# Kernel optimization log

Measured on AMD Instinct MI355X. Metric: run time of the kernel, lower is better.

The kernel has to match this reference:

```python
import jax, jax.numpy as jnp
import numpy as np

B, T, C, HP, WP = 2, 8, 384, 128, 128
WS = 8
NH = 12  # num_heads
EPS = 1e-5


def setup_inputs() -> dict:
    key = jax.random.key(0)
    ks = jax.random.split(key, 9)
    s = 0.02
    return {
        "x": jax.random.normal(ks[0], (B, T, C, HP, WP), jnp.float32),
        "norm_gamma": jnp.ones((C,), jnp.float32),
        "norm_beta": jnp.zeros((C,), jnp.float32),
        "in_proj_w": jax.random.normal(ks[1], (3 * C, C), jnp.float32) * s,
        "in_proj_b": jnp.zeros((3 * C,), jnp.float32),
        "out_proj_w": jax.random.normal(ks[2], (C, C), jnp.float32) * s,
        "out_proj_b": jnp.zeros((C,), jnp.float32),
        "proj_w": jax.random.normal(ks[3], (C, C), jnp.float32) * s,
        "proj_b": jnp.zeros((C,), jnp.float32),
    }


def reference(x, norm_gamma, norm_beta, in_proj_w, in_proj_b,
              out_proj_w, out_proj_b, proj_w, proj_b):
    b, t, c, hp, wp = x.shape
    ws = WS
    nh, nw = hp // ws, wp // ws
    dh = c // NH

    # window partition: (B,T,C,H,W) -> (B*T*nH*nW, ws*ws, C)
    xw = jnp.transpose(x, (0, 1, 3, 4, 2))                # (B,T,H,W,C)
    xw = xw.reshape(b * t, nh, ws, nw, ws, c)
    xw = jnp.transpose(xw, (0, 1, 3, 2, 4, 5))            # (BT,nH,nW,ws,ws,C)
    xw = xw.reshape(b * t * nh * nw, ws * ws, c)          # (N,S,C)

    # LayerNorm over channel dim
    mu = jnp.mean(xw, axis=-1, keepdims=True)
    var = jnp.mean((xw - mu) ** 2, axis=-1, keepdims=True)
    xn = (xw - mu) * jax.lax.rsqrt(var + EPS) * norm_gamma + norm_beta

    # fused QKV projection (torch MHA in_proj layout: rows are [q;k;v])
    qkv = jnp.einsum('nsc,dc->nsd', xn, in_proj_w) + in_proj_b
    q, k, v = jnp.split(qkv, 3, axis=-1)
    n, s = q.shape[0], q.shape[1]
    q = q.reshape(n, s, NH, dh)
    k = k.reshape(n, s, NH, dh)
    v = v.reshape(n, s, NH, dh)

    scale = 1.0 / np.sqrt(dh).astype(np.float32)
    attn = jnp.einsum('nqhd,nkhd->nhqk', q * scale, k)
    attn = jax.nn.softmax(attn, axis=-1)
    o = jnp.einsum('nhqk,nkhd->nqhd', attn, v).reshape(n, s, c)

    # MHA out_proj then extra proj
    o = jnp.einsum('nsc,dc->nsd', o, out_proj_w) + out_proj_b
    o = jnp.einsum('nsc,dc->nsd', o, proj_w) + proj_b

    # window merge back to (B,T,C,H,W)
    o = o.reshape(b * t, nh, nw, ws, ws, c)
    o = jnp.transpose(o, (0, 1, 3, 2, 4, 5)).reshape(b, t, hp, wp, c)
    return jnp.transpose(o, (0, 1, 4, 2, 3))
```

## Files before the change

### kernel.cpp

```cpp
#include <hip/hip_runtime.h>

#define C_    384
#define NH_   12
#define DH_   32
#define HPX   128
#define WPX   128
#define NWIN_ 4096
#define TOK_  262144

typedef __attribute__((ext_vector_type(8))) short short8;
typedef __attribute__((ext_vector_type(4))) float f32x4;

__device__ __forceinline__ unsigned short f2bf(float f) {
  unsigned u = __builtin_bit_cast(unsigned, f);
  u = (u + 0x7fffu + ((u >> 16) & 1u)) >> 16;
  return (unsigned short)u;
}

__global__ __launch_bounds__(256) void prep_kernel(
    const float* __restrict__ in_w, const float* __restrict__ op_w,
    const float* __restrict__ op_b, const float* __restrict__ p_w,
    const float* __restrict__ p_b, unsigned short* __restrict__ wqkv,
    unsigned short* __restrict__ wf, float* __restrict__ bfv)
{
  int tid = blockIdx.x * blockDim.x + threadIdx.x;
  int stride = gridDim.x * blockDim.x;
  for (int i = tid; i < 3 * C_ * C_; i += stride) wqkv[i] = f2bf(in_w[i]);
  for (int i = tid; i < C_ * C_; i += stride) {
    int r = i / C_, c = i % C_;
    float acc = 0.f;
    for (int k = 0; k < C_; k++) acc += p_w[r * C_ + k] * op_w[k * C_ + c];
    wf[i] = f2bf(acc);
  }
  for (int i = tid; i < C_; i += stride) {
    float acc = p_b[i];
    for (int k = 0; k < C_; k++) acc += p_w[i * C_ + k] * op_b[k];
    bfv[i] = acc;
  }
}

__global__ __launch_bounds__(256) void fused_attn(
    const float* __restrict__ x, const float* __restrict__ gamma,
    const float* __restrict__ beta, const unsigned short* __restrict__ wqkv,
    const float* __restrict__ bqkv, unsigned short* __restrict__ o1)
{
  __shared__ char smem[61440];
  char* xnb = smem;
  char* Qb  = smem + 49152;
  char* Kb  = smem + 53248;
  char* VTb = smem + 57344;
  char* Pb  = smem + 49152;
  float* red   = (float*)(smem + 49152);
  float* stats = (float*)(smem + 49152 + 2048);

  const int win = (blockIdx.x & 7) * (NWIN_ / 8) + (blockIdx.x >> 3);
  const int bt = win >> 8, wh = (win >> 4) & 15, ww = win & 15;
  const int tid = threadIdx.x;
  const int w = tid >> 6, l = tid & 63;
  const int l15 = l & 15, sub = l >> 4;

  const float* xb = x + ((size_t)bt * C_ * HPX + (size_t)wh * 8) * WPX + ww * 8;
  const int i0 = l >> 3, j0 = l & 7;

  float sm = 0.f, sq = 0.f;
  for (int c = w; c < C_; c += 4) {
    float v = xb[(size_t)c * (HPX * WPX) + i0 * WPX + j0];
    sm += v; sq += v * v;
  }
  red[(w * 64 + l) * 2] = sm;
  red[(w * 64 + l) * 2 + 1] = sq;
  __syncthreads();
  if (tid < 64) {
    float a0 = 0.f, a1 = 0.f;
    for (int p = 0; p < 4; p++) { a0 += red[(p * 64 + tid) * 2]; a1 += red[(p * 64 + tid) * 2 + 1]; }
    float mu = a0 * (1.f / C_);
    float var = a1 * (1.f / C_) - mu * mu;
    stats[tid * 2] = mu;
    stats[tid * 2 + 1] = rsqrtf(var + 1e-5f);
  }
  __syncthreads();
  const float mu = stats[l * 2], rsg = stats[l * 2 + 1];

  for (int c = w; c < C_; c += 4) {
    float v = xb[(size_t)c * (HPX * WPX) + i0 * WPX + j0];
    float xv = (v - mu) * rsg * gamma[c] + beta[c];
    unsigned byte = (unsigned)(l * 768 + c * 2) ^ (unsigned)((l & 7) << 4);
    *(unsigned short*)(xnb + byte) = f2bf(xv);
  }
  __syncthreads();

  const int mw = w >> 1, nw = w & 1;
  const float scale = 0.1767766952966369f;
  const f32x4 zf = {0.f, 0.f, 0.f, 0.f};

  for (int h = 0; h < NH_; h++) {
    int wr[3];
    #pragma unroll
    for (int jj = 0; jj < 3; jj++) {
      int j = 3 * nw + jj;
      wr[jj] = (j >> 1) * C_ + h * DH_ + (j & 1) * 16;
    }
    f32x4 acc[2][3];
    #pragma unroll
    for (int r = 0; r < 2; r++)
      #pragma unroll
      for (int jj = 0; jj < 3; jj++) acc[r][jj] = zf;

    for (int kc = 0; kc < 12; kc++) {
      short8 a[2];
      #pragma unroll
      for (int r = 0; r < 2; r++) {
        int tok = 32 * mw + 16 * r + l15;
        unsigned byte = (unsigned)(tok * 768 + kc * 64 + (sub << 4)) ^ (unsigned)((tok & 7) << 4);
        a[r] = *(const short8*)(xnb + byte);
      }
      #pragma unroll
      for (int jj = 0; jj < 3; jj++) {
        short8 b = *(const short8*)(wqkv + ((size_t)(wr[jj] + l15) * C_ + kc * 32 + (sub << 3)));
        acc[0][jj] = __builtin_amdgcn_mfma_f32_16x16x32_bf16(a[0], b, acc[0][jj], 0, 0, 0);
        acc[1][jj] = __builtin_amdgcn_mfma_f32_16x16x32_bf16(a[1], b, acc[1][jj], 0, 0, 0);
      }
    }
    __syncthreads();

    #pragma unroll
    for (int jj = 0; jj < 3; jj++) {
      int j = 3 * nw + jj;
      int typ = j >> 1;
      int dloc = (j & 1) * 16 + l15;
      float bias = bqkv[wr[jj] + l15];
      #pragma unroll
      for (int r = 0; r < 2; r++) {
        #pragma unroll
        for (int rr = 0; rr < 4; rr++) {
          int tok = 32 * mw + 16 * r + (sub << 2) + rr;
          float v = acc[r][jj][rr] + bias;
          if (typ == 0) {
            v *= scale;
            unsigned byte = (unsigned)(tok * 64 + dloc * 2) ^ (unsigned)((tok & 7) << 4);
            *(unsigned short*)(Qb + byte) = f2bf(v);
          } else if (typ == 1) {
            unsigned byte = (unsigned)(tok * 64 + dloc * 2) ^ (unsigned)((tok & 7) << 4);
            *(unsigned short*)(Kb + byte) = f2bf(v);
          } else {
            unsigned byte = (unsigned)(dloc * 128 + tok * 2) ^ (unsigned)((dloc & 7) << 4);
            *(unsigned short*)(VTb + byte) = f2bf(v);
          }
        }
      }
    }
    __syncthreads();

    short8 qa;
    {
      int tok = 16 * w + l15;
      unsigned byte = (unsigned)(tok * 64 + (sub << 4)) ^ (unsigned)((tok & 7) << 4);
      qa = *(const short8*)(Qb + byte);
    }
    f32x4 sacc[4];
    #pragma unroll
    for (int ct = 0; ct < 4; ct++) {
      int kt = ct * 16 + l15;
      unsigned byte = (unsigned)(kt * 64 + (sub << 4)) ^ (unsigned)((kt & 7) << 4);
      short8 kb = *(const short8*)(Kb + byte);
      sacc[ct] = __builtin_amdgcn_mfma_f32_16x16x32_bf16(qa, kb, zf, 0, 0, 0);
    }
    float inv[4];
    #pragma unroll
    for (int rr = 0; rr < 4; rr++) {
      float m = fmaxf(fmaxf(sacc[0][rr], sacc[1][rr]), fmaxf(sacc[2][rr], sacc[3][rr]));
      m = fmaxf(m, __shfl_xor(m, 1));
      m = fmaxf(m, __shfl_xor(m, 2));
      m = fmaxf(m, __shfl_xor(m, 4));
      m = fmaxf(m, __shfl_xor(m, 8));
      float s = 0.f;
      #pragma unroll
      for (int ct = 0; ct < 4; ct++) {
        float p = __expf(sacc[ct][rr] - m);
        sacc[ct][rr] = p;
        s += p;
      }
      s += __shfl_xor(s, 1); s += __shfl_xor(s, 2);
      s += __shfl_xor(s, 4); s += __shfl_xor(s, 8);
      inv[rr] = 1.0f / s;
    }
    __syncthreads();
    #pragma unroll
    for (int ct = 0; ct < 4; ct++)
      #pragma unroll
      for (int rr = 0; rr < 4; rr++) {
        int q = 16 * w + (sub << 2) + rr;
        int kk = ct * 16 + l15;
        unsigned byte = (unsigned)(q * 128 + kk * 2) ^ (unsigned)((q & 7) << 4);
        *(unsigned short*)(Pb + byte) = f2bf(sacc[ct][rr]);
      }
    __syncthreads();

    f32x4 oacc[2] = {zf, zf};
    #pragma unroll
    for (int kc = 0; kc < 2; kc++) {
      int q = 16 * w + l15;
      unsigned pb = (unsigned)(q * 128 + kc * 64 + (sub << 4)) ^ (unsigned)((q & 7) << 4);
      short8 pa = *(const short8*)(Pb + pb);
      #pragma unroll
      for (int dt = 0; dt < 2; dt++) {
        int d = dt * 16 + l15;
        unsigned vb = (unsigned)(d * 128 + kc * 64 + (sub << 4)) ^ (unsigned)((d & 7) << 4);
        short8 vv = *(const short8*)(VTb + vb);
        oacc[dt] = __builtin_amdgcn_mfma_f32_16x16x32_bf16(pa, vv, oacc[dt], 0, 0, 0);
      }
    }
    #pragma unroll
    for (int dt = 0; dt < 2; dt++)
      #pragma unroll
      for (int rr = 0; rr < 4; rr++) {
        int q = 16 * w + (sub << 2) + rr;
        int col = h * DH_ + dt * 16 + l15;
        o1[(size_t)(win * 64 + q) * C_ + col] = f2bf(oacc[dt][rr] * inv[rr]);
      }
  }
}

__global__ __launch_bounds__(256) void final_gemm(
    const unsigned short* __restrict__ o1, const unsigned short* __restrict__ wf,
    const float* __restrict__ bfv, float* __restrict__ out)
{
  __shared__ char smem[32768];
  char* As = smem;
  char* Bs = smem + 16384;

  const int blk = blockIdx.x;
  const int nt = blk % 3, mt = blk / 3;
  const int mbase = mt * 128, nbase = nt * 128;
  const int tid = threadIdx.x;
  const int w = tid >> 6, l = tid & 63;
  const int l15 = l & 15, sub = l >> 4;
  const int wm = w >> 1, wn = w & 1;
  const f32x4 zf = {0.f, 0.f, 0.f, 0.f};

  f32x4 acc[4][4];
  #pragma unroll
  for (int r = 0; r < 4; r++)
    #pragma unroll
    for (int c = 0; c < 4; c++) acc[r][c] = zf;

  for (int kb = 0; kb < C_; kb += 64) {
    __syncthreads();
    #pragma unroll
    for (int it = 0; it < 4; it++) {
      int row = it * 32 + (tid >> 3);
      int seg = tid & 7;
      unsigned byte = (unsigned)(row * 128 + seg * 16) ^ (unsigned)((row & 7) << 4);
      short8 va = *(const short8*)(o1 + (size_t)(mbase + row) * C_ + kb + seg * 8);
      *(short8*)(As + byte) = va;
      short8 vb = *(const short8*)(wf + (size_t)(nbase + row) * C_ + kb + seg * 8);
      *(short8*)(Bs + byte) = vb;
    }
    __syncthreads();
    #pragma unroll
    for (int kc = 0; kc < 2; kc++) {
      short8 a[4], b[4];
      #pragma unroll
      for (int r = 0; r < 4; r++) {
        int row = wm * 64 + r * 16 + l15;
        unsigned byte = (unsigned)(row * 128 + kc * 64 + (sub << 4)) ^ (unsigned)((row & 7) << 4);
        a[r] = *(const short8*)(As + byte);
      }
      #pragma unroll
      for (int c = 0; c < 4; c++) {
        int row = wn * 64 + c * 16 + l15;
        unsigned byte = (unsigned)(row * 128 + kc * 64 + (sub << 4)) ^ (unsigned)((row & 7) << 4);
        b[c] = *(const short8*)(Bs + byte);
      }
      #pragma unroll
      for (int r = 0; r < 4; r++)
        #pragma unroll
        for (int c = 0; c < 4; c++)
          acc[r][c] = __builtin_amdgcn_mfma_f32_16x16x32_bf16(a[r], b[c], acc[r][c], 0, 0, 0);
    }
  }

  #pragma unroll
  for (int r = 0; r < 4; r++) {
    int t0 = mbase + wm * 64 + r * 16 + (sub << 2);
    int win = t0 >> 6, s0 = t0 & 63;
    int bt = win >> 8, wh = (win >> 4) & 15, ww = win & 15;
    int ii = s0 >> 3, jj = s0 & 7;
    #pragma unroll
    for (int c4 = 0; c4 < 4; c4++) {
      int c = nbase + wn * 64 + c4 * 16 + l15;
      float bias = bfv[c];
      f32x4 v;
      v[0] = acc[r][c4][0] + bias;
      v[1] = acc[r][c4][1] + bias;
      v[2] = acc[r][c4][2] + bias;
      v[3] = acc[r][c4][3] + bias;
      size_t off = (((size_t)bt * C_ + c) * HPX + wh * 8 + ii) * WPX + ww * 8 + jj;
      *(f32x4*)(out + off) = v;
    }
  }
}

extern "C" void kernel_launch(void* const* d_in, const int* in_sizes, int n_in,
                              void* d_out, int out_size, void* d_ws, size_t ws_size,
                              hipStream_t stream)
{
  (void)in_sizes; (void)n_in; (void)out_size; (void)ws_size;
  const float* x     = (const float*)d_in[0];
  const float* gamma = (const float*)d_in[1];
  const float* beta  = (const float*)d_in[2];
  const float* in_w  = (const float*)d_in[3];
  const float* in_b  = (const float*)d_in[4];
  const float* op_w  = (const float*)d_in[5];
  const float* op_b  = (const float*)d_in[6];
  const float* p_w   = (const float*)d_in[7];
  const float* p_b   = (const float*)d_in[8];
  float* out = (float*)d_out;
  char* ws = (char*)d_ws;

  const size_t o1_bytes = (size_t)TOK_ * C_ * 2;
  unsigned short* o1   = (unsigned short*)ws;
  unsigned short* wqkv = (unsigned short*)(ws + o1_bytes);
  unsigned short* wf   = (unsigned short*)(ws + o1_bytes + 884736);
  float*          bfv  = (float*)(ws + o1_bytes + 884736 + 294912);

  prep_kernel<<<1024, 256, 0, stream>>>(in_w, op_w, op_b, p_w, p_b, wqkv, wf, bfv);
  fused_attn<<<NWIN_, 256, 0, stream>>>(x, gamma, beta, wqkv, in_b, o1);
  final_gemm<<<2048 * 3, 256, 0, stream>>>(o1, wf, bfv, out);
}
```

Baseline: 2.186 ms.

## Split fused window attention into LN, tiled QKV GEMM, and per-window attention kernels

Replaces the single fused LN+QKV+attention kernel with three stages: a LayerNorm/window-partition kernel writing bf16 xn to workspace, a 128x128 LDS-tiled QKV GEMM writing Q (pre-scaled), K and transposed V, and a per-window attention kernel that reads them from global memory. The goal is to remove the per-head GEMM in the fused kernel that re-read weights straight from global memory without LDS tiling, and to raise occupancy. The work is processed in chunks sized to fit the workspace, and attention output overwrites xn in place. The cost is extra global round-trips for xn and QKV and possibly many kernel launches when the workspace is small.

New measurement: 1.883 ms. 13.9% less time.

```diff
diff --git a/kernel.cpp b/kernel.cpp
--- a/kernel.cpp
+++ b/kernel.cpp
@@ -39,17 +39,12 @@
   }
 }
 
-__global__ __launch_bounds__(256) void fused_attn(
+__global__ __launch_bounds__(256) void ln_win(
     const float* __restrict__ x, const float* __restrict__ gamma,
-    const float* __restrict__ beta, const unsigned short* __restrict__ wqkv,
-    const float* __restrict__ bqkv, unsigned short* __restrict__ o1)
-{
-  __shared__ char smem[61440];
+    const float* __restrict__ beta, unsigned short* __restrict__ xn)
+{
+  __shared__ char smem[51712];
   char* xnb = smem;
-  char* Qb  = smem + 49152;
-  char* Kb  = smem + 53248;
-  char* VTb = smem + 57344;
-  char* Pb  = smem + 49152;
   float* red   = (float*)(smem + 49152);
   float* stats = (float*)(smem + 49152 + 2048);
 
@@ -57,15 +52,15 @@
   const int bt = win >> 8, wh = (win >> 4) & 15, ww = win & 15;
   const int tid = threadIdx.x;
   const int w = tid >> 6, l = tid & 63;
-  const int l15 = l & 15, sub = l >> 4;
-
   const float* xb = x + ((size_t)bt * C_ * HPX + (size_t)wh * 8) * WPX + ww * 8;
-  const int i0 = l >> 3, j0 = l & 7;
+  const int px = (l >> 3) * WPX + (l & 7);
 
   float sm = 0.f, sq = 0.f;
-  for (int c = w; c < C_; c += 4) {
-    float v = xb[(size_t)c * (HPX * WPX) + i0 * WPX + j0];
-    sm += v; sq += v * v;
+  for (int cp = w; cp < 192; cp += 4) {
+    int c = cp * 2;
+    float v0 = xb[(size_t)c * (HPX * WPX) + px];
+    float v1 = xb[(size_t)(c + 1) * (HPX * WPX) + px];
+    sm += v0 + v1; sq += v0 * v0 + v1 * v1;
   }
   red[(w * 64 + l) * 2] = sm;
   red[(w * 64 + l) * 2 + 1] = sq;
@@ -81,149 +76,225 @@
   __syncthreads();
   const float mu = stats[l * 2], rsg = stats[l * 2 + 1];
 
-  for (int c = w; c < C_; c += 4) {
-    float v = xb[(size_t)c * (HPX * WPX) + i0 * WPX + j0];
-    float xv = (v - mu) * rsg * gamma[c] + beta[c];
+  for (int cp = w; cp < 192; cp += 4) {
+    int c = cp * 2;
+    float v0 = xb[(size_t)c * (HPX * WPX) + px];
+    float v1 = xb[(size_t)(c + 1) * (HPX * WPX) + px];
+    float y0 = (v0 - mu) * rsg * gamma[c] + beta[c];
+    float y1 = (v1 - mu) * rsg * gamma[c + 1] + beta[c + 1];
+    unsigned pk = (unsigned)f2bf(y0) | ((unsigned)f2bf(y1) << 16);
     unsigned byte = (unsigned)(l * 768 + c * 2) ^ (unsigned)((l & 7) << 4);
-    *(unsigned short*)(xnb + byte) = f2bf(xv);
+    *(unsigned*)(xnb + byte) = pk;
   }
   __syncthreads();
 
-  const int mw = w >> 1, nw = w & 1;
+  unsigned short* xg = xn + (size_t)win * (64 * C_);
+  #pragma unroll
+  for (int i = 0; i < 12; i++) {
+    unsigned g = (unsigned)(i * 4096 + tid * 16);
+    unsigned row = g / 768;
+    unsigned byte = g ^ ((row & 7) << 4);
+    short8 v = *(const short8*)(xnb + byte);
+    *(short8*)(xg + (g >> 1)) = v;
+  }
+}
+
+__global__ __launch_bounds__(256) void qkv_gemm(
+    const unsigned short* __restrict__ xn, const unsigned short* __restrict__ wqkv,
+    const float* __restrict__ bqkv, unsigned short* __restrict__ qs,
+    unsigned short* __restrict__ ksp, unsigned short* __restrict__ vt)
+{
+  __shared__ char smem[32768];
+  char* As = smem;
+  char* Bs = smem + 16384;
+
+  const int blk = blockIdx.x;
+  const int nt = blk % 9, mt = blk / 9;
+  const int mbase = mt * 128, nbase = nt * 128;
+  const int tid = threadIdx.x;
+  const int w = tid >> 6, l = tid & 63;
+  const int l15 = l & 15, sub = l >> 4;
+  const int wm = w >> 1, wn = w & 1;
+  const f32x4 zf = {0.f, 0.f, 0.f, 0.f};
   const float scale = 0.1767766952966369f;
+
+  f32x4 acc[4][4];
+  #pragma unroll
+  for (int r = 0; r < 4; r++)
+    #pragma unroll
+    for (int c = 0; c < 4; c++) acc[r][c] = zf;
+
+  for (int kb = 0; kb < C_; kb += 64) {
+    __syncthreads();
+    #pragma unroll
+    for (int it = 0; it < 4; it++) {
+      int row = it * 32 + (tid >> 3);
+      int seg = tid & 7;
+      unsigned byte = (unsigned)(row * 128 + seg * 16) ^ (unsigned)((row & 7) << 4);
+      short8 va = *(const short8*)(xn + (size_t)(mbase + row) * C_ + kb + seg * 8);
+      *(short8*)(As + byte) = va;
+      short8 vb = *(const short8*)(wqkv + (size_t)(nbase + row) * C_ + kb + seg * 8);
+      *(short8*)(Bs + byte) = vb;
+    }
+    __syncthreads();
+    #pragma unroll
+    for (int kc = 0; kc < 2; kc++) {
+      short8 a[4], b[4];
+      #pragma unroll
+      for (int r = 0; r < 4; r++) {
+        int row = wm * 64 + r * 16 + l15;
+        unsigned byte = (unsigned)(row * 128 + kc * 64 + (sub << 4)) ^ (unsigned)((row & 7) << 4);
+        a[r] = *(const short8*)(As + byte);
+      }
+      #pragma unroll
+      for (int c = 0; c < 4; c++) {
+        int row = wn * 64 + c * 16 + l15;
+        unsigned byte = (unsigned)(row * 128 + kc * 64 + (sub << 4)) ^ (unsigned)((row & 7) << 4);
+        b[c] = *(const short8*)(Bs + byte);
+      }
+      #pragma unroll
+      for (int r = 0; r < 4; r++)
+        #pragma unroll
+        for (int c = 0; c < 4; c++)
+          acc[r][c] = __builtin_amdgcn_mfma_f32_16x16x32_bf16(a[r], b[c], acc[r][c], 0, 0, 0);
+    }
+  }
+
+  const int typ = nt / 3;
+  #pragma unroll
+  for (int r = 0; r < 4; r++) {
+    int t0 = mbase + wm * 64 + r * 16 + (sub << 2);
+    #pragma unroll
+    for (int c4 = 0; c4 < 4; c4++) {
+      int dg = nbase + wn * 64 + c4 * 16 + l15;
+      float bias = bqkv[dg];
+      if (typ == 0) {
+        #pragma unroll
+        for (int reg = 0; reg < 4; reg++)
+          qs[(size_t)(t0 + reg) * C_ + dg] = f2bf((acc[r][c4][reg] + bias) * scale);
+      } else if (typ == 1) {
+        #pragma unroll
+        for (int reg = 0; reg < 4; reg++)
+          ksp[(size_t)(t0 + reg) * C_ + (dg - C_)] = f2bf(acc[r][c4][reg] + bias);
+      } else {
+        int vd = dg - 2 * C_;
+        int win_l = t0 >> 6, s0 = t0 & 63;
+        unsigned short b0 = f2bf(acc[r][c4][0] + bias);
+        unsigned short b1 = f2bf(acc[r][c4][1] + bias);
+        unsigned short b2 = f2bf(acc[r][c4][2] + bias);
+        unsigned short b3 = f2bf(acc[r][c4][3] + bias);
+        unsigned lo = (unsigned)b0 | ((unsigned)b1 << 16);
+        unsigned hi = (unsigned)b2 | ((unsigned)b3 << 16);
+        unsigned* p = (unsigned*)(vt + ((size_t)win_l * C_ + vd) * 64 + s0);
+        p[0] = lo; p[1] = hi;
+      }
+    }
+  }
+}
+
+__global__ __launch_bounds__(256, 4) void attn_win(
+    const unsigned short* __restrict__ qs, const unsigned short* __restrict__ ksp,
+    const unsigned short* __restrict__ vt, unsigned short* __restrict__ o1)
+{
+  __shared__ char Pall[32768];
+  const int win_l = blockIdx.x;
+  const int tid = threadIdx.x;
+  const int w = tid >> 6, l = tid & 63;
+  const int l15 = l & 15, sub = l >> 4;
+  char* Pb = Pall + w * 8192;
+  const unsigned short* qw = qs + (size_t)win_l * 64 * C_;
+  const unsigned short* kw = ksp + (size_t)win_l * 64 * C_;
+  const unsigned short* vw = vt + (size_t)win_l * C_ * 64;
+  unsigned short* ow = o1 + (size_t)win_l * 64 * C_;
   const f32x4 zf = {0.f, 0.f, 0.f, 0.f};
 
-  for (int h = 0; h < NH_; h++) {
-    int wr[3];
-    #pragma unroll
-    for (int jj = 0; jj < 3; jj++) {
-      int j = 3 * nw + jj;
-      wr[jj] = (j >> 1) * C_ + h * DH_ + (j & 1) * 16;
-    }
-    f32x4 acc[2][3];
-    #pragma unroll
-    for (int r = 0; r < 2; r++)
-      #pragma unroll
-      for (int jj = 0; jj < 3; jj++) acc[r][jj] = zf;
-
-    for (int kc = 0; kc < 12; kc++) {
-      short8 a[2];
-      #pragma unroll
-      for (int r = 0; r < 2; r++) {
-        int tok = 32 * mw + 16 * r + l15;
-        unsigned byte = (unsigned)(tok * 768 + kc * 64 + (sub << 4)) ^ (unsigned)((tok & 7) << 4);
-        a[r] = *(const short8*)(xnb + byte);
-      }
-      #pragma unroll
-      for (int jj = 0; jj < 3; jj++) {
-        short8 b = *(const short8*)(wqkv + ((size_t)(wr[jj] + l15) * C_ + kc * 32 + (sub << 3)));
-        acc[0][jj] = __builtin_amdgcn_mfma_f32_16x16x32_bf16(a[0], b, acc[0][jj], 0, 0, 0);
-        acc[1][jj] = __builtin_amdgcn_mfma_f32_16x16x32_bf16(a[1], b, acc[1][jj], 0, 0, 0);
-      }
-    }
-    __syncthreads();
-
-    #pragma unroll
-    for (int jj = 0; jj < 3; jj++) {
-      int j = 3 * nw + jj;
-      int typ = j >> 1;
-      int dloc = (j & 1) * 16 + l15;
-      float bias = bqkv[wr[jj] + l15];
-      #pragma unroll
-      for (int r = 0; r < 2; r++) {
-        #pragma unroll
-        for (int rr = 0; rr < 4; rr++) {
-          int tok = 32 * mw + 16 * r + (sub << 2) + rr;
-          float v = acc[r][jj][rr] + bias;
-          if (typ == 0) {
-            v *= scale;
-            unsigned byte = (unsigned)(tok * 64 + dloc * 2) ^ (unsigned)((tok & 7) << 4);
-            *(unsigned short*)(Qb + byte) = f2bf(v);
-          } else if (typ == 1) {
-            unsigned byte = (unsigned)(tok * 64 + dloc * 2) ^ (unsigned)((tok & 7) << 4);
-            *(unsigned short*)(Kb + byte) = f2bf(v);
-          } else {
-            unsigned byte = (unsigned)(dloc * 128 + tok * 2) ^ (unsigned)((dloc & 7) << 4);
-            *(unsigned short*)(VTb + byte) = f2bf(v);
+  for (int hh = 0; hh < 3; hh++) {
+    const int h = w + hh * 4;
+    short8 kf[4];
+    #pragma unroll
+    for (int ct = 0; ct < 4; ct++)
+      kf[ct] = *(const short8*)(kw + (size_t)(ct * 16 + l15) * C_ + h * DH_ + sub * 8);
+
+    #pragma unroll
+    for (int hf = 0; hf < 2; hf++) {
+      f32x4 sc[2][4];
+      #pragma unroll
+      for (int rt2 = 0; rt2 < 2; rt2++) {
+        int rt = hf * 2 + rt2;
+        short8 qf = *(const short8*)(qw + (size_t)(rt * 16 + l15) * C_ + h * DH_ + sub * 8);
+        #pragma unroll
+        for (int ct = 0; ct < 4; ct++)
+          sc[rt2][ct] = __builtin_amdgcn_mfma_f32_16x16x32_bf16(qf, kf[ct], zf, 0, 0, 0);
+      }
+      float inv[2][4];
+      #pragma unroll
+      for (int rt2 = 0; rt2 < 2; rt2++) {
+        #pragma unroll
+        for (int reg = 0; reg < 4; reg++) {
+          float m = fmaxf(fmaxf(sc[rt2][0][reg], sc[rt2][1][reg]),
+                          fmaxf(sc[rt2][2][reg], sc[rt2][3][reg]));
+          m = fmaxf(m, __shfl_xor(m, 1));
+          m = fmaxf(m, __shfl_xor(m, 2));
+          m = fmaxf(m, __shfl_xor(m, 4));
+          m = fmaxf(m, __shfl_xor(m, 8));
+          float s = 0.f;
+          #pragma unroll
+          for (int ct = 0; ct < 4; ct++) {
+            float p = __expf(sc[rt2][ct][reg] - m);
+            sc[rt2][ct][reg] = p;
+            s += p;
           }
+          s += __shfl_xor(s, 1); s += __shfl_xor(s, 2);
+          s += __shfl_xor(s, 4); s += __shfl_xor(s, 8);
+          inv[rt2][reg] = 1.0f / s;
         }
       }
-    }
-    __syncthreads();
-
-    short8 qa;
-    {
-      int tok = 16 * w + l15;
-      unsigned byte = (unsigned)(tok * 64 + (sub << 4)) ^ (unsigned)((tok & 7) << 4);
-      qa = *(const short8*)(Qb + byte);
-    }
-    f32x4 sacc[4];
-    #pragma unroll
-    for (int ct = 0; ct < 4; ct++) {
-      int kt = ct * 16 + l15;
-      unsigned byte = (unsigned)(kt * 64 + (sub << 4)) ^ (unsigned)((kt & 7) << 4);
-      short8 kb = *(const short8*)(Kb + byte);
-      sacc[ct] = __builtin_amdgcn_mfma_f32_16x16x32_bf16(qa, kb, zf, 0, 0, 0);
-    }
-    float inv[4];
-    #pragma unroll
-    for (int rr = 0; rr < 4; rr++) {
-      float m = fmaxf(fmaxf(sacc[0][rr], sacc[1][rr]), fmaxf(sacc[2][rr], sacc[3][rr]));
-      m = fmaxf(m, __shfl_xor(m, 1));
-      m = fmaxf(m, __shfl_xor(m, 2));
-      m = fmaxf(m, __shfl_xor(m, 4));
-      m = fmaxf(m, __shfl_xor(m, 8));
-      float s = 0.f;
-      #pragma unroll
-      for (int ct = 0; ct < 4; ct++) {
-        float p = __expf(sacc[ct][rr] - m);
-        sacc[ct][rr] = p;
-        s += p;
-      }
-      s += __shfl_xor(s, 1); s += __shfl_xor(s, 2);
-      s += __shfl_xor(s, 4); s += __shfl_xor(s, 8);
-      inv[rr] = 1.0f / s;
-    }
-    __syncthreads();
-    #pragma unroll
-    for (int ct = 0; ct < 4; ct++)
-      #pragma unroll
-      for (int rr = 0; rr < 4; rr++) {
-        int q = 16 * w + (sub << 2) + rr;
-        int kk = ct * 16 + l15;
-        unsigned byte = (unsigned)(q * 128 + kk * 2) ^ (unsigned)((q & 7) << 4);
-        *(unsigned short*)(Pb + byte) = f2bf(sacc[ct][rr]);
-      }
-    __syncthreads();
-
-    f32x4 oacc[2] = {zf, zf};
-    #pragma unroll
-    for (int kc = 0; kc < 2; kc++) {
-      int q = 16 * w + l15;
-      unsigned pb = (unsigned)(q * 128 + kc * 64 + (sub << 4)) ^ (unsigned)((q & 7) << 4);
-      short8 pa = *(const short8*)(Pb + pb);
-      #pragma unroll
-      for (int dt = 0; dt < 2; dt++) {
-        int d = dt * 16 + l15;
-        unsigned vb = (unsigned)(d * 128 + kc * 64 + (sub << 4)) ^ (unsigned)((d & 7) << 4);
-        short8 vv = *(const short8*)(VTb + vb);
-        oacc[dt] = __builtin_amdgcn_mfma_f32_16x16x32_bf16(pa, vv, oacc[dt], 0, 0, 0);
-      }
-    }
-    #pragma unroll
-    for (int dt = 0; dt < 2; dt++)
-      #pragma unroll
-      for (int rr = 0; rr < 4; rr++) {
-        int q = 16 * w + (sub << 2) + rr;
-        int col = h * DH_ + dt * 16 + l15;
-        o1[(size_t)(win * 64 + q) * C_ + col] = f2bf(oacc[dt][rr] * inv[rr]);
-      }
+      #pragma unroll
+      for (int rt2 = 0; rt2 < 2; rt2++)
+        #pragma unroll
+        for (int ct = 0; ct < 4; ct++)
+          #pragma unroll
+          for (int reg = 0; reg < 4; reg++) {
+            int q = (hf * 2 + rt2) * 16 + (sub << 2) + reg;
+            int k = ct * 16 + l15;
+            unsigned byte = (unsigned)(q * 128 + k * 2) ^ (unsigned)((q & 7) << 4);
+            *(unsigned short*)(Pb + byte) = f2bf(sc[rt2][ct][reg]);
+          }
+      f32x4 oa[2][2] = {{zf, zf}, {zf, zf}};
+      #pragma unroll
+      for (int kc = 0; kc < 2; kc++) {
+        short8 pa[2];
+        #pragma unroll
+        for (int rt2 = 0; rt2 < 2; rt2++) {
+          int q = (hf * 2 + rt2) * 16 + l15;
+          unsigned byte = (unsigned)(q * 128 + kc * 64 + (sub << 4)) ^ (unsigned)((q & 7) << 4);
+          pa[rt2] = *(const short8*)(Pb + byte);
+        }
+        #pragma unroll
+        for (int dt = 0; dt < 2; dt++) {
+          short8 b = *(const short8*)(vw + (size_t)(h * DH_ + dt * 16 + l15) * 64 + kc * 32 + sub * 8);
+          #pragma unroll
+          for (int rt2 = 0; rt2 < 2; rt2++)
+            oa[rt2][dt] = __builtin_amdgcn_mfma_f32_16x16x32_bf16(pa[rt2], b, oa[rt2][dt], 0, 0, 0);
+        }
+      }
+      #pragma unroll
+      for (int rt2 = 0; rt2 < 2; rt2++)
+        #pragma unroll
+        for (int dt = 0; dt < 2; dt++)
+          #pragma unroll
+          for (int reg = 0; reg < 4; reg++) {
+            int q = (hf * 2 + rt2) * 16 + (sub << 2) + reg;
+            ow[(size_t)q * C_ + h * DH_ + dt * 16 + l15] =
+                f2bf(oa[rt2][dt][reg] * inv[rt2][reg]);
+          }
+    }
   }
 }
 
 __global__ __launch_bounds__(256) void final_gemm(
     const unsigned short* __restrict__ o1, const unsigned short* __restrict__ wf,
-    const float* __restrict__ bfv, float* __restrict__ out)
+    const float* __restrict__ bfv, float* __restrict__ out, int winBase)
 {
   __shared__ char smem[32768];
   char* As = smem;
@@ -283,7 +354,7 @@
   #pragma unroll
   for (int r = 0; r < 4; r++) {
     int t0 = mbase + wm * 64 + r * 16 + (sub << 2);
-    int win = t0 >> 6, s0 = t0 & 63;
+    int win = winBase + (t0 >> 6), s0 = t0 & 63;
     int bt = win >> 8, wh = (win >> 4) & 15, ww = win & 15;
     int ii = s0 >> 3, jj = s0 & 7;
     #pragma unroll
@@ -305,7 +376,7 @@
                               void* d_out, int out_size, void* d_ws, size_t ws_size,
                               hipStream_t stream)
 {
-  (void)in_sizes; (void)n_in; (void)out_size; (void)ws_size;
+  (void)in_sizes; (void)n_in; (void)out_size;
   const float* x     = (const float*)d_in[0];
   const float* gamma = (const float*)d_in[1];
   const float* beta  = (const float*)d_in[2];
@@ -318,13 +389,41 @@
   float* out = (float*)d_out;
   char* ws = (char*)d_ws;
 
-  const size_t o1_bytes = (size_t)TOK_ * C_ * 2;
-  unsigned short* o1   = (unsigned short*)ws;
-  unsigned short* wqkv = (unsigned short*)(ws + o1_bytes);
-  unsigned short* wf   = (unsigned short*)(ws + o1_bytes + 884736);
-  float*          bfv  = (float*)(ws + o1_bytes + 884736 + 294912);
+  const size_t XN_B   = (size_t)TOK_ * C_ * 2;
+  const size_t QKV_B  = (size_t)TOK_ * 3 * C_ * 2;
+  const size_t WQKV_B = (size_t)3 * C_ * C_ * 2;
+  const size_t WF_B   = (size_t)C_ * C_ * 2;
+  const size_t BF_B   = 2048;
+
+  const int cand[9] = {1, 2, 4, 8, 16, 32, 64, 128, 256};
+  int nchunks = 256;
+  for (int i = 0; i < 9; i++) {
+    size_t need = XN_B + QKV_B / (size_t)cand[i] + WQKV_B + WF_B + BF_B;
+    if (need <= ws_size) { nchunks = cand[i]; break; }
+  }
+  const int chunkWins = NWIN_ / nchunks;
+  const size_t chunkTok = (size_t)chunkWins * 64;
+  const size_t qkv_slab = QKV_B / (size_t)nchunks;
+
+  unsigned short* xn   = (unsigned short*)ws;
+  char* qbase          = ws + XN_B;
+  unsigned short* wqkv = (unsigned short*)(ws + XN_B + qkv_slab);
+  unsigned short* wf   = (unsigned short*)(ws + XN_B + qkv_slab + WQKV_B);
+  float*          bfv  = (float*)(ws + XN_B + qkv_slab + WQKV_B + WF_B);
+
+  unsigned short* qs  = (unsigned short*)qbase;
+  unsigned short* ksp = qs + chunkTok * C_;
+  unsigned short* vt  = ksp + chunkTok * C_;
 
   prep_kernel<<<1024, 256, 0, stream>>>(in_w, op_w, op_b, p_w, p_b, wqkv, wf, bfv);
-  fused_attn<<<NWIN_, 256, 0, stream>>>(x, gamma, beta, wqkv, in_b, o1);
-  final_gemm<<<2048 * 3, 256, 0, stream>>>(o1, wf, bfv, out);
-}
+  ln_win<<<NWIN_, 256, 0, stream>>>(x, gamma, beta, xn);
+
+  const int mtiles = (int)(chunkTok / 128);
+  for (int c = 0; c < nchunks; c++) {
+    const int winBase = c * chunkWins;
+    unsigned short* xn_c = xn + (size_t)winBase * 64 * C_;
+    qkv_gemm<<<mtiles * 9, 256, 0, stream>>>(xn_c, wqkv, in_b, qs, ksp, vt);
+    attn_win<<<chunkWins, 256, 0, stream>>>(qs, ksp, vt, xn_c);
+    final_gemm<<<mtiles * 3, 256, 0, stream>>>(xn_c, wf, bfv, out, winBase);
+  }
+}
```
